# Optimization experiments

Measured on AMD Instinct MI355X. Metric: run time of the kernel, lower is better.

The kernel has to match this reference:

```python
import jax, jax.numpy as jnp
import numpy as np
import math

B, L, HID = 2, 2048, 1024
NH, DH = 16, 64
MASK_VAL = -1000000000.0  # half_precision_flag == False


def setup_inputs() -> dict:
    key = jax.random.key(0)
    ks = jax.random.split(key, 12)
    s = 0.02
    return {
        "queries": jax.random.normal(ks[0], (B, L, HID), jnp.float32),
        "keys": jax.random.normal(ks[1], (B, L, HID), jnp.float32),
        "values": jax.random.normal(ks[2], (B, L, HID), jnp.float32),
        "mask": jax.random.randint(ks[3], (B, L, L), 0, 2, jnp.int32),
        "Wq": jax.random.normal(ks[4], (HID, NH * DH), jnp.float32) * s,
        "bq": jnp.zeros((NH * DH,), jnp.float32),
        "Wk": jax.random.normal(ks[5], (HID, NH * DH), jnp.float32) * s,
        "bk": jnp.zeros((NH * DH,), jnp.float32),
        "Wv": jax.random.normal(ks[6], (HID, NH * DH), jnp.float32) * s,
        "bv": jnp.zeros((NH * DH,), jnp.float32),
        "Wo": jax.random.normal(ks[7], (NH * DH, HID), jnp.float32) * s,
        "bo": jnp.zeros((HID,), jnp.float32),
    }


def reference(queries, keys, values, mask, Wq, bq, Wk, bk, Wv, bv, Wo, bo):
    # Linear projections: (B, L, NH*DH)
    q = queries @ Wq + bq
    k = keys @ Wk + bk
    v = values @ Wv + bv
    # FAITHFUL to original: raw .view(B, NH, -1, DH) without transpose
    q = q.reshape(B, NH, L, DH)
    k = k.reshape(B, NH, L, DH)
    v = v.reshape(B, NH, L, DH)
    # scaled dot-product scores: (B, NH, L, L)
    scores = jnp.einsum("bhqd,bhkd->bhqk", q, k) / math.sqrt(DH)
    scores = jnp.where(mask[:, None, :, :] == 0, MASK_VAL, scores)
    probs = jax.nn.softmax(scores, axis=-1)  # dropout p=0 -> identity
    ctx = jnp.einsum("bhqk,bhkd->bhqd", probs, v)  # (B, NH, L, DH)
    # transpose(1,2) then flatten heads, as in original
    ctx = ctx.transpose(0, 2, 1, 3).reshape(B, L, NH * DH)
    return ctx @ Wo + bo
```

## Files before the change

kernel.cpp:

```cpp
#include <hip/hip_runtime.h>
#include <stdint.h>

typedef __bf16 bf16;
typedef __bf16 bf16x8 __attribute__((ext_vector_type(8)));
typedef __bf16 bf16x4 __attribute__((ext_vector_type(4)));
typedef float  f32x4  __attribute__((ext_vector_type(4)));
typedef short  s16x4  __attribute__((ext_vector_type(4)));
typedef unsigned long long ull;

#define GLOAD16(gptr, lptr)                                                     \
  __builtin_amdgcn_global_load_lds(                                             \
      (const __attribute__((address_space(1))) void*)(gptr),                    \
      (__attribute__((address_space(3))) void*)(lptr), 16, 0, 0)

#define MFMA16(a, b, c) __builtin_amdgcn_mfma_f32_16x16x32_bf16((a), (b), (c), 0, 0, 0)
#define MFMA16K16(a, b, c) __builtin_amdgcn_mfma_f32_16x16x16bf16_1k((a), (b), (c), 0, 0, 0)

static constexpr int B_ = 2, L_ = 2048, NH_ = 16, DH_ = 64;
static constexpr float QSCALE = 0.18033688011112042f;

__global__ void k_cvt3(const float* __restrict__ q, const float* __restrict__ k,
                       const float* __restrict__ v, bf16* __restrict__ outbase) {
  const float* in = blockIdx.y == 0 ? q : (blockIdx.y == 1 ? k : v);
  bf16* out = outbase + (size_t)blockIdx.y * 4194304;
  int i = blockIdx.x * blockDim.x + threadIdx.x;
  const float4 f = ((const float4*)in)[i];
  bf16x4 o = {(bf16)f.x, (bf16)f.y, (bf16)f.z, (bf16)f.w};
  ((bf16x4*)out)[i] = o;
}

__global__ void k_wtrans4(const float* __restrict__ wq, const float* __restrict__ wk,
                          const float* __restrict__ wv, const float* __restrict__ wo,
                          bf16* __restrict__ outbase) {
  const int z = blockIdx.z;
  const float* in = z == 0 ? wq : (z == 1 ? wk : (z == 2 ? wv : wo));
  bf16* out = outbase + (size_t)z * 1048576;
  __shared__ float t[32][33];
  int bx = blockIdx.x * 32, by = blockIdx.y * 32;
  int x = threadIdx.x & 31, y = threadIdx.x >> 5;
#pragma unroll
  for (int r = 0; r < 4; ++r)
    t[y + r * 8][x] = in[(size_t)(by + y + r * 8) * 1024 + bx + x];
  __syncthreads();
#pragma unroll
  for (int r = 0; r < 4; ++r)
    out[(size_t)(bx + y + r * 8) * 1024 + by + x] = (bf16)t[x][y + r * 8];
}

__global__ void k_maskbits(const int* __restrict__ mask, ull* __restrict__ mb) {
  int t = blockIdx.x * blockDim.x + threadIdx.x;
  ull bal = __ballot(mask[t] != 0);
  if ((threadIdx.x & 63) == 0) mb[t >> 6] = bal;
}

__global__ __launch_bounds__(256) void k_gemm3(const bf16* __restrict__ Xb,
                                               const bf16* __restrict__ Wb,
                                               const float* __restrict__ b0,
                                               const float* __restrict__ b1,
                                               const float* __restrict__ b2,
                                               bf16* __restrict__ Ob) {
  const int z = blockIdx.z;
  const bf16* A  = Xb + (size_t)z * 4194304;
  const bf16* Bt = Wb + (size_t)z * 1048576;
  const float* bias = z == 0 ? b0 : (z == 1 ? b1 : b2);
  bf16* C = Ob + (size_t)z * 4194304;
  const int m0 = blockIdx.y * 128, n0 = blockIdx.x * 128;
  __shared__ __align__(16) bf16 As[128 * 32];
  __shared__ __align__(16) bf16 Bs[128 * 32];
  const int tid = threadIdx.x, lane = tid & 63, w = tid >> 6, quad = lane >> 4, l15 = lane & 15;
  const int wm = (w & 1) * 64, wn = (w >> 1) * 64;
  f32x4 acc[4][4] = {};
  for (int kt = 0; kt < 32; ++kt) {
    const int kk = kt * 32;
#pragma unroll
    for (int i = 0; i < 2; ++i) {
      int s = tid + i * 256;
      int r = s >> 2, c = (s & 3) ^ ((r >> 1) & 3);
      GLOAD16(A + (size_t)(m0 + r) * 1024 + kk + c * 8, As + s * 8);
      GLOAD16(Bt + (size_t)(n0 + r) * 1024 + kk + c * 8, Bs + s * 8);
    }
    __syncthreads();
    bf16x8 af[4], bb[4];
#pragma unroll
    for (int i = 0; i < 4; ++i) {
      int ra = wm + i * 16 + l15, rb = wn + i * 16 + l15;
      af[i] = *(const bf16x8*)(As + (ra * 4 + (quad ^ ((ra >> 1) & 3))) * 8);
      bb[i] = *(const bf16x8*)(Bs + (rb * 4 + (quad ^ ((rb >> 1) & 3))) * 8);
    }
#pragma unroll
    for (int mi = 0; mi < 4; ++mi)
#pragma unroll
      for (int ni = 0; ni < 4; ++ni)
        acc[mi][ni] = MFMA16(af[mi], bb[ni], acc[mi][ni]);
    __syncthreads();
  }
  const float scale = (z == 0) ? QSCALE : 1.0f;
#pragma unroll
  for (int mi = 0; mi < 4; ++mi)
#pragma unroll
    for (int ni = 0; ni < 4; ++ni) {
      int row = m0 + wm + mi * 16 + quad * 4;
      int col = n0 + wn + ni * 16 + l15;
      float bz = bias[col];
      if (z == 2) {
        int b_ = row >> 11, l = row & 2047;
        int hh = l >> 7;
        int i0 = (l & 127) * 16 + (col >> 6);
        int d  = col & 63;
        bf16* dst = C + (size_t)(b_ * 16 + hh) * 131072;
#pragma unroll
        for (int r = 0; r < 4; ++r) {
          int iK = i0 + 16 * r;
          dst[((size_t)(iK >> 2) * 64 + d) * 4 + (iK & 3)] = (bf16)(acc[mi][ni][r] + bz);
        }
      } else {
#pragma unroll
        for (int r = 0; r < 4; ++r)
          C[(size_t)(row + r) * 1024 + col] = (bf16)((acc[mi][ni][r] + bz) * scale);
      }
    }
}

__global__ __launch_bounds__(256) void k_gemmo(const bf16* __restrict__ A,
                                               const bf16* __restrict__ Bt,
                                               const float* __restrict__ bias,
                                               float* __restrict__ C) {
  const int m0 = blockIdx.y * 64, n0 = blockIdx.x * 128;
  __shared__ __align__(16) bf16 As[64 * 32];
  __shared__ __align__(16) bf16 Bs[128 * 32];
  const int tid = threadIdx.x, lane = tid & 63, w = tid >> 6, quad = lane >> 4, l15 = lane & 15;
  const int wn = w * 32;
  f32x4 acc[4][2] = {};
  for (int kt = 0; kt < 32; ++kt) {
    const int kk = kt * 32;
    {
      int r = tid >> 2, c = (tid & 3) ^ ((r >> 1) & 3);
      GLOAD16(A + (size_t)(m0 + r) * 1024 + kk + c * 8, As + tid * 8);
    }
#pragma unroll
    for (int i = 0; i < 2; ++i) {
      int s = tid + i * 256;
      int r = s >> 2, c = (s & 3) ^ ((r >> 1) & 3);
      GLOAD16(Bt + (size_t)(n0 + r) * 1024 + kk + c * 8, Bs + s * 8);
    }
    __syncthreads();
    bf16x8 af[4], bb[2];
#pragma unroll
    for (int i = 0; i < 4; ++i) {
      int ra = i * 16 + l15;
      af[i] = *(const bf16x8*)(As + (ra * 4 + (quad ^ ((ra >> 1) & 3))) * 8);
    }
#pragma unroll
    for (int i = 0; i < 2; ++i) {
      int rb = wn + i * 16 + l15;
      bb[i] = *(const bf16x8*)(Bs + (rb * 4 + (quad ^ ((rb >> 1) & 3))) * 8);
    }
#pragma unroll
    for (int mi = 0; mi < 4; ++mi)
#pragma unroll
      for (int ni = 0; ni < 2; ++ni)
        acc[mi][ni] = MFMA16(af[mi], bb[ni], acc[mi][ni]);
    __syncthreads();
  }
#pragma unroll
  for (int mi = 0; mi < 4; ++mi)
#pragma unroll
    for (int ni = 0; ni < 2; ++ni) {
      int row = m0 + mi * 16 + quad * 4;
      int col = n0 + wn + ni * 16 + l15;
      float bz = bias[col];
#pragma unroll
      for (int r = 0; r < 4; ++r)
        C[(size_t)(row + r) * 1024 + col] = acc[mi][ni][r] + bz;
    }
}

__global__ __launch_bounds__(256) void k_flash(const bf16* __restrict__ Qp,
                                               const bf16* __restrict__ Kp,
                                               const bf16* __restrict__ Vtp,
                                               const ull* __restrict__ mb,
                                               bf16* __restrict__ ctx) {
  const int b = blockIdx.z, h = blockIdx.y, q0 = blockIdx.x * 128;
  const size_t HEAD = 131072;
  const bf16* Q  = Qp  + ((size_t)b * NH_ + h) * HEAD;
  const bf16* K  = Kp  + ((size_t)b * NH_ + h) * HEAD;
  const bf16* Vt = Vtp + ((size_t)b * NH_ + h) * HEAD;
  const ull* mrow = mb + (size_t)b * L_ * 32;

  __shared__ __align__(16) bf16 Ks[2][64 * 64];
  __shared__ __align__(16) bf16 Vs[2][64 * 64];
  __shared__ __align__(16) ull  Ms[2][256];

  const int tid = threadIdx.x, lane = tid & 63, w = tid >> 6, quad = lane >> 4, l15 = lane & 15;

  bf16x8 qf[2][2];
#pragma unroll
  for (int qb = 0; qb < 2; ++qb)
#pragma unroll
    for (int ks = 0; ks < 2; ++ks)
      qf[qb][ks] = *(const bf16x8*)(Q + (size_t)(q0 + w * 32 + qb * 16 + l15) * 64 + ks * 32 + quad * 8);

#pragma unroll
  for (int i = 0; i < 2; ++i) {
    int s = tid + i * 256;
    int key = s >> 3, c = (s & 7) ^ (key & 7);
    GLOAD16(K + (size_t)key * 64 + c * 8, Ks[0] + s * 8);
    GLOAD16(Vt + (size_t)s * 8, Vs[0] + s * 8);
  }
  if (w < 2) {
    int r = w * 64 + lane;
    GLOAD16(mrow + (size_t)(q0 + r) * 32, (bf16*)&Ms[0][0] + r * 8);
  }
  __syncthreads();

  f32x4 accO[2][4] = {};
  float lsum[2] = {0.f, 0.f};

  for (int kt = 0; kt < 32; ++kt) {
    const int cur = kt & 1;
    if (kt + 1 < 32) {
      const int nxt = cur ^ 1;
#pragma unroll
      for (int i = 0; i < 2; ++i) {
        int s = tid + i * 256;
        int key = s >> 3, c = (s & 7) ^ (key & 7);
        GLOAD16(K + (size_t)((kt + 1) * 64 + key) * 64 + c * 8, Ks[nxt] + s * 8);
        GLOAD16(Vt + (size_t)(kt + 1) * 4096 + s * 8, Vs[nxt] + s * 8);
      }
      if ((kt & 1) && w < 2) {
        int r = w * 64 + lane;
        GLOAD16(mrow + (size_t)(q0 + r) * 32 + (kt + 1),
                (bf16*)&Ms[((kt + 1) >> 1) & 1][0] + r * 8);
      }
    }

    f32x4 st[4][2] = {};
#pragma unroll
    for (int ks = 0; ks < 2; ++ks)
#pragma unroll
      for (int kb = 0; kb < 4; ++kb) {
        int key = kb * 16 + l15;
        bf16x8 kf = *(const bf16x8*)(Ks[cur] + (key * 8 + ((ks * 4 + quad) ^ (key & 7))) * 8);
        st[kb][0] = MFMA16(kf, qf[0][ks], st[kb][0]);
        st[kb][1] = MFMA16(kf, qf[1][ks], st[kb][1]);
      }

    const ull* Mcur = Ms[(kt >> 1) & 1];
    const ull word0 = Mcur[(w * 32 + l15) * 2 + cur];
    const ull word1 = Mcur[(w * 32 + 16 + l15) * 2 + cur];
    s16x4 pf[4][2];
#pragma unroll
    for (int kb = 0; kb < 4; ++kb)
#pragma unroll
      for (int qb = 0; qb < 2; ++qb) {
        const unsigned nib = (unsigned)((qb ? word1 : word0) >> (kb * 16 + quad * 4)) & 0xFu;
        float p0 = (nib & 1u) ? __builtin_amdgcn_exp2f(st[kb][qb][0]) : 0.f;
        float p1 = (nib & 2u) ? __builtin_amdgcn_exp2f(st[kb][qb][1]) : 0.f;
        float p2 = (nib & 4u) ? __builtin_amdgcn_exp2f(st[kb][qb][2]) : 0.f;
        float p3 = (nib & 8u) ? __builtin_amdgcn_exp2f(st[kb][qb][3]) : 0.f;
        lsum[qb] += (p0 + p1) + (p2 + p3);
        bf16x4 pb = {(bf16)p0, (bf16)p1, (bf16)p2, (bf16)p3};
        pf[kb][qb] = __builtin_bit_cast(s16x4, pb);
      }

#pragma unroll
    for (int kb = 0; kb < 4; ++kb)
#pragma unroll
      for (int db = 0; db < 4; ++db) {
        s16x4 vf = *(const s16x4*)(Vs[cur] + ((size_t)((kb * 4 + quad) * 64 + db * 16 + l15)) * 4);
        accO[0][db] = MFMA16K16(pf[kb][0], vf, accO[0][db]);
        accO[1][db] = MFMA16K16(pf[kb][1], vf, accO[1][db]);
      }
    __syncthreads();
  }

#pragma unroll
  for (int qb = 0; qb < 2; ++qb) {
    lsum[qb] += __shfl_xor(lsum[qb], 16, 64);
    lsum[qb] += __shfl_xor(lsum[qb], 32, 64);
  }
#pragma unroll
  for (int qb = 0; qb < 2; ++qb) {
    float rl[4];
#pragma unroll
    for (int r = 0; r < 4; ++r)
      rl[r] = 1.0f / __shfl(lsum[qb], quad * 4 + r, 64);
#pragma unroll
    for (int db = 0; db < 4; ++db) {
      const int col = h * 64 + db * 16 + l15;
#pragma unroll
      for (int r = 0; r < 4; ++r) {
        const int rowg = q0 + w * 32 + qb * 16 + quad * 4 + r;
        ctx[((size_t)b * L_ + rowg) * 1024 + col] = (bf16)(accO[qb][db][r] * rl[r]);
      }
    }
  }
}

extern "C" void kernel_launch(void* const* d_in, const int* in_sizes, int n_in,
                              void* d_out, int out_size, void* d_ws, size_t ws_size,
                              hipStream_t stream) {
  (void)in_sizes; (void)n_in; (void)out_size; (void)ws_size;
  const float* q    = (const float*)d_in[0];
  const float* k    = (const float*)d_in[1];
  const float* v    = (const float*)d_in[2];
  const int*   mask = (const int*)d_in[3];
  const float* Wq = (const float*)d_in[4];
  const float* bq = (const float*)d_in[5];
  const float* Wk = (const float*)d_in[6];
  const float* bk = (const float*)d_in[7];
  const float* Wv = (const float*)d_in[8];
  const float* bv = (const float*)d_in[9];
  const float* Wo = (const float*)d_in[10];
  const float* bo = (const float*)d_in[11];
  float* out = (float*)d_out;

  char* ws = (char*)d_ws;
  const size_t SX = (size_t)4096 * 1024 * 2;
  const size_t SW = (size_t)1024 * 1024 * 2;
  bf16* X   = (bf16*)(ws);
  bf16* Wt  = (bf16*)(ws + 3 * SX);
  bf16* QKV = (bf16*)(ws + 3 * SX + 4 * SW);
  bf16* Qp  = QKV;
  bf16* Kp  = QKV + 4194304;
  bf16* Vtp = QKV + 2 * 4194304;
  bf16* Ctx = (bf16*)(ws + 6 * SX + 4 * SW);
  ull* mbits = (ull*)(ws + 7 * SX + 4 * SW);

  dim3 blk(256);
  k_cvt3<<<dim3(4096, 3), blk, 0, stream>>>(q, k, v, X);
  k_wtrans4<<<dim3(32, 32, 4), blk, 0, stream>>>(Wq, Wk, Wv, Wo, Wt);
  k_maskbits<<<32768, blk, 0, stream>>>(mask, mbits);

  k_gemm3<<<dim3(8, 32, 3), blk, 0, stream>>>(X, Wt, bq, bk, bv, QKV);

  k_flash<<<dim3(16, NH_, B_), blk, 0, stream>>>(Qp, Kp, Vtp, mbits, Ctx);

  k_gemmo<<<dim3(8, 64), blk, 0, stream>>>(Ctx, Wt + 3 * 1048576, bo, out);
}
```

Before: 280.4 us.

## Merge prep kernels, read V directly from global, compute row sums via MFMA

Fuses the three preprocessing kernels (input conversion, weight transpose, mask bit-packing) into one launch that dispatches on block index, removing two launch overheads. In the flash kernel, the V tile is no longer staged through LDS; each lane loads its V fragments straight from global memory. The softmax row sum now comes from an extra MFMA against a ones vector instead of scalar adds plus cross-lane shuffles. Reading V from global puts memory latency on the MFMA path with no double buffering, while the ones-MFMA adds matrix work but removes VALU adds and shuffles.

```diff
diff --git a/kernel.cpp b/kernel.cpp
--- a/kernel.cpp
+++ b/kernel.cpp
@@ -19,38 +19,47 @@
 static constexpr int B_ = 2, L_ = 2048, NH_ = 16, DH_ = 64;
 static constexpr float QSCALE = 0.18033688011112042f;
 
-__global__ void k_cvt3(const float* __restrict__ q, const float* __restrict__ k,
-                       const float* __restrict__ v, bf16* __restrict__ outbase) {
-  const float* in = blockIdx.y == 0 ? q : (blockIdx.y == 1 ? k : v);
-  bf16* out = outbase + (size_t)blockIdx.y * 4194304;
-  int i = blockIdx.x * blockDim.x + threadIdx.x;
-  const float4 f = ((const float4*)in)[i];
-  bf16x4 o = {(bf16)f.x, (bf16)f.y, (bf16)f.z, (bf16)f.w};
-  ((bf16x4*)out)[i] = o;
-}
-
-__global__ void k_wtrans4(const float* __restrict__ wq, const float* __restrict__ wk,
-                          const float* __restrict__ wv, const float* __restrict__ wo,
-                          bf16* __restrict__ outbase) {
-  const int z = blockIdx.z;
-  const float* in = z == 0 ? wq : (z == 1 ? wk : (z == 2 ? wv : wo));
-  bf16* out = outbase + (size_t)z * 1048576;
+__global__ __launch_bounds__(256) void k_prep(const float* __restrict__ q,
+                                              const float* __restrict__ k,
+                                              const float* __restrict__ v,
+                                              const int* __restrict__ mask,
+                                              const float* __restrict__ wq,
+                                              const float* __restrict__ wk,
+                                              const float* __restrict__ wv,
+                                              const float* __restrict__ wo,
+                                              bf16* __restrict__ X,
+                                              bf16* __restrict__ Wt,
+                                              ull* __restrict__ mb) {
   __shared__ float t[32][33];
-  int bx = blockIdx.x * 32, by = blockIdx.y * 32;
-  int x = threadIdx.x & 31, y = threadIdx.x >> 5;
-#pragma unroll
-  for (int r = 0; r < 4; ++r)
-    t[y + r * 8][x] = in[(size_t)(by + y + r * 8) * 1024 + bx + x];
-  __syncthreads();
-#pragma unroll
-  for (int r = 0; r < 4; ++r)
-    out[(size_t)(bx + y + r * 8) * 1024 + by + x] = (bf16)t[x][y + r * 8];
-}
-
-__global__ void k_maskbits(const int* __restrict__ mask, ull* __restrict__ mb) {
-  int t = blockIdx.x * blockDim.x + threadIdx.x;
-  ull bal = __ballot(mask[t] != 0);
-  if ((threadIdx.x & 63) == 0) mb[t >> 6] = bal;
+  const int bid = blockIdx.x, tid = threadIdx.x;
+  if (bid < 32768) {
+    int tt = bid * 256 + tid;
+    ull bal = __ballot(mask[tt] != 0);
+    if ((tid & 63) == 0) mb[tt >> 6] = bal;
+  } else if (bid < 45056) {
+    int u = bid - 32768;
+    int z = u >> 12, x = u & 4095;
+    const float* in = z == 0 ? q : (z == 1 ? k : v);
+    bf16* out = X + (size_t)z * 4194304;
+    int i = x * 256 + tid;
+    const float4 f = ((const float4*)in)[i];
+    bf16x4 o = {(bf16)f.x, (bf16)f.y, (bf16)f.z, (bf16)f.w};
+    ((bf16x4*)out)[i] = o;
+  } else {
+    int u = bid - 45056;
+    int z = u >> 10, rem = u & 1023;
+    const float* in = z == 0 ? wq : (z == 1 ? wk : (z == 2 ? wv : wo));
+    bf16* out = Wt + (size_t)z * 1048576;
+    int bx = (rem & 31) * 32, by = (rem >> 5) * 32;
+    int x = tid & 31, y = tid >> 5;
+#pragma unroll
+    for (int r = 0; r < 4; ++r)
+      t[y + r * 8][x] = in[(size_t)(by + y + r * 8) * 1024 + bx + x];
+    __syncthreads();
+#pragma unroll
+    for (int r = 0; r < 4; ++r)
+      out[(size_t)(bx + y + r * 8) * 1024 + by + x] = (bf16)t[x][y + r * 8];
+  }
 }
 
 __global__ __launch_bounds__(256) void k_gemm3(const bf16* __restrict__ Xb,
@@ -188,7 +197,6 @@
   const ull* mrow = mb + (size_t)b * L_ * 32;
 
   __shared__ __align__(16) bf16 Ks[2][64 * 64];
-  __shared__ __align__(16) bf16 Vs[2][64 * 64];
   __shared__ __align__(16) ull  Ms[2][256];
 
   const int tid = threadIdx.x, lane = tid & 63, w = tid >> 6, quad = lane >> 4, l15 = lane & 15;
@@ -205,7 +213,6 @@
     int s = tid + i * 256;
     int key = s >> 3, c = (s & 7) ^ (key & 7);
     GLOAD16(K + (size_t)key * 64 + c * 8, Ks[0] + s * 8);
-    GLOAD16(Vt + (size_t)s * 8, Vs[0] + s * 8);
   }
   if (w < 2) {
     int r = w * 64 + lane;
@@ -214,7 +221,8 @@
   __syncthreads();
 
   f32x4 accO[2][4] = {};
-  float lsum[2] = {0.f, 0.f};
+  f32x4 accL[2] = {};
+  const s16x4 onesf = {0x3F80, 0x3F80, 0x3F80, 0x3F80};
 
   for (int kt = 0; kt < 32; ++kt) {
     const int cur = kt & 1;
@@ -225,7 +233,6 @@
         int s = tid + i * 256;
         int key = s >> 3, c = (s & 7) ^ (key & 7);
         GLOAD16(K + (size_t)((kt + 1) * 64 + key) * 64 + c * 8, Ks[nxt] + s * 8);
-        GLOAD16(Vt + (size_t)(kt + 1) * 4096 + s * 8, Vs[nxt] + s * 8);
       }
       if ((kt & 1) && w < 2) {
         int r = w * 64 + lane;
@@ -258,33 +265,37 @@
         float p1 = (nib & 2u) ? __builtin_amdgcn_exp2f(st[kb][qb][1]) : 0.f;
         float p2 = (nib & 4u) ? __builtin_amdgcn_exp2f(st[kb][qb][2]) : 0.f;
         float p3 = (nib & 8u) ? __builtin_amdgcn_exp2f(st[kb][qb][3]) : 0.f;
-        lsum[qb] += (p0 + p1) + (p2 + p3);
         bf16x4 pb = {(bf16)p0, (bf16)p1, (bf16)p2, (bf16)p3};
         pf[kb][qb] = __builtin_bit_cast(s16x4, pb);
       }
 
 #pragma unroll
-    for (int kb = 0; kb < 4; ++kb)
+    for (int kb = 0; kb < 4; ++kb) {
+      accL[0] = MFMA16K16(pf[kb][0], onesf, accL[0]);
+      accL[1] = MFMA16K16(pf[kb][1], onesf, accL[1]);
+    }
+
+#pragma unroll
+    for (int kb = 0; kb < 4; ++kb) {
+      s16x4 vf[4];
+#pragma unroll
+      for (int db = 0; db < 4; ++db)
+        vf[db] = *(const s16x4*)(Vt + (size_t)kt * 4096 +
+                                 ((size_t)((kb * 4 + quad) * 64 + db * 16 + l15)) * 4);
 #pragma unroll
       for (int db = 0; db < 4; ++db) {
-        s16x4 vf = *(const s16x4*)(Vs[cur] + ((size_t)((kb * 4 + quad) * 64 + db * 16 + l15)) * 4);
-        accO[0][db] = MFMA16K16(pf[kb][0], vf, accO[0][db]);
-        accO[1][db] = MFMA16K16(pf[kb][1], vf, accO[1][db]);
-      }
-    __syncthreads();
-  }
-
-#pragma unroll
-  for (int qb = 0; qb < 2; ++qb) {
-    lsum[qb] += __shfl_xor(lsum[qb], 16, 64);
-    lsum[qb] += __shfl_xor(lsum[qb], 32, 64);
-  }
+        accO[0][db] = MFMA16K16(pf[kb][0], vf[db], accO[0][db]);
+        accO[1][db] = MFMA16K16(pf[kb][1], vf[db], accO[1][db]);
+      }
+    }
+    __syncthreads();
+  }
+
 #pragma unroll
   for (int qb = 0; qb < 2; ++qb) {
     float rl[4];
 #pragma unroll
-    for (int r = 0; r < 4; ++r)
-      rl[r] = 1.0f / __shfl(lsum[qb], quad * 4 + r, 64);
+    for (int r = 0; r < 4; ++r) rl[r] = 1.0f / accL[qb][r];
 #pragma unroll
     for (int db = 0; db < 4; ++db) {
       const int col = h * 64 + db * 16 + l15;
@@ -328,9 +339,7 @@
   ull* mbits = (ull*)(ws + 7 * SX + 4 * SW);
 
   dim3 blk(256);
-  k_cvt3<<<dim3(4096, 3), blk, 0, stream>>>(q, k, v, X);
-  k_wtrans4<<<dim3(32, 32, 4), blk, 0, stream>>>(Wq, Wk, Wv, Wo, Wt);
-  k_maskbits<<<32768, blk, 0, stream>>>(mask, mbits);
+  k_prep<<<49152, blk, 0, stream>>>(q, k, v, mask, Wq, Wk, Wv, Wo, X, Wt, mbits);
 
   k_gemm3<<<dim3(8, 32, 3), blk, 0, stream>>>(X, Wt, bq, bk, bv, QKV);
 
```

Result: slower. 295.0 us (+5.2%).
